# Optimization experiments

Hardware: AMD Instinct MI355X
Metric: run time of the kernel (lower is better)

The kernel has to match this reference:

```python
import jax, jax.numpy as jnp
import numpy as np
from jax.scipy.special import gammaln

N_L, N_Q, D_IN, D_CTX, H, MAX_AGENT = 256, 65536, 384, 192, 64, 6
STD2 = 0.1
VAR2 = STD2 * STD2
LOG_VAR2 = float(np.log(VAR2))
TEMP = 1.0


def _linear_init(k, out_dim, in_dim):
    k1, k2 = jax.random.split(k)
    s = 1.0 / np.sqrt(in_dim)
    w = jax.random.uniform(k1, (out_dim, in_dim), minval=-s, maxval=s, dtype=jnp.float32)
    b = jax.random.uniform(k2, (out_dim,), minval=-s, maxval=s, dtype=jnp.float32)
    return w, b


def setup_inputs() -> dict:
    key = jax.random.key(0)
    ks = jax.random.split(key, 12)
    fc1_w, fc1_b = _linear_init(ks[0], H, D_IN)
    fc21_w, fc21_b = _linear_init(ks[1], H, H)
    fc22_w, fc22_b = _linear_init(ks[2], H, H)
    fc3_w, fc3_b = _linear_init(ks[3], H, H)
    fc4_w, fc4_b = _linear_init(ks[4], D_IN, H)
    ctx_w, ctx_b = _linear_init(ks[5], H, D_CTX)
    llms = jax.random.normal(ks[6], (N_L, D_IN), dtype=jnp.float32)
    contexts = jax.random.normal(ks[7], (N_Q, D_CTX), dtype=jnp.float32)
    agent_num_int = jax.random.randint(ks[8], (N_Q, 1), 1, MAX_AGENT + 1, dtype=jnp.int32)
    agent_num_float = agent_num_int.astype(jnp.float32)
    noise_eps = jax.random.normal(ks[9], (N_L, H), dtype=jnp.float32)   # VAE reparameterize eps
    rand_u = jax.random.uniform(ks[10], (MAX_AGENT, N_Q, 1), dtype=jnp.float32)  # per-step uniforms
    return dict(llms=llms, contexts=contexts, agent_num_int=agent_num_int,
                agent_num_float=agent_num_float,
                fc1_w=fc1_w, fc1_b=fc1_b, fc21_w=fc21_w, fc21_b=fc21_b,
                fc22_w=fc22_w, fc22_b=fc22_b, fc3_w=fc3_w, fc3_b=fc3_b,
                fc4_w=fc4_w, fc4_b=fc4_b, ctx_w=ctx_w, ctx_b=ctx_b,
                noise_eps=noise_eps, rand_u=rand_u)


def _l2norm(x):
    n = jnp.sqrt(jnp.sum(x * x, axis=1, keepdims=True))
    return x / jnp.maximum(n, 1e-12)


def reference(llms, contexts, agent_num_int, agent_num_float,
              fc1_w, fc1_b, fc21_w, fc21_b, fc22_w, fc22_b,
              fc3_w, fc3_b, fc4_w, fc4_b, ctx_w, ctx_b, noise_eps, rand_u):
    # ---- VAE encode / reparameterize / decode ----
    h = jax.nn.relu(llms @ fc1_w.T + fc1_b)
    mu = h @ fc21_w.T + fc21_b
    log_var = h @ fc22_w.T + fc22_b
    std = jnp.exp(0.5 * log_var) * STD2
    z = mu + noise_eps * std
    h2 = jax.nn.relu(z @ fc3_w.T + fc3_b)
    x_hat = h2 @ fc4_w.T + fc4_b
    mse = jnp.mean((x_hat - llms) ** 2)
    kld = -0.5 * jnp.mean(1.0 - LOG_VAR2 + log_var - (mu ** 2 + jnp.exp(log_var)) / VAR2)
    vae_loss = mse + kld

    # ---- embeddings and routing scores ----
    llm_emb = _l2norm(z)                                   # [N_l, H]
    ctx_emb = _l2norm(contexts @ ctx_w.T + ctx_b)          # [N_q, H]
    scores = jax.nn.softmax((ctx_emb @ llm_emb.T) / TEMP, axis=1)  # [N_q, N_l]
    scores_cumsum = jnp.cumsum(scores, axis=1)

    # ---- vectorized max_agent-step categorical sampling ----
    # sel[i, q] = first llm where cumsum > u (inverse-CDF sampling), for step i
    sel = jnp.argmax(scores_cumsum[None, :, :] > rand_u, axis=2)          # [A, N_q]
    steps = jnp.arange(1, rand_u.shape[0] + 1, dtype=agent_num_int.dtype)
    mask = (agent_num_int[None, :, 0] >= steps[:, None]).astype(scores.dtype)  # [A, N_q]
    rows = jnp.broadcast_to(jnp.arange(scores.shape[0])[None, :], sel.shape)
    selected_llm = jnp.zeros_like(scores).at[rows, sel].add(mask)          # [N_q, N_l]

    log_probs = (gammaln(agent_num_float + 1.0)
                 - jnp.sum(gammaln(selected_llm + 1.0), axis=1, keepdims=True)
                 + jnp.sum(selected_llm * jnp.log(scores), axis=1, keepdims=True))
    return selected_llm, log_probs, vae_loss
```

## Files before the change

### kernel.cpp

```cpp
#include <hip/hip_runtime.h>
#include <hip/hip_bf16.h>

#define N_L 256
#define N_Q 65536
#define D_IN 384
#define D_CTX 192
#define HDIM 64
#define MAXA 6

__device__ __forceinline__ void fma4(float& acc, const float4& w, const float4& v) {
    acc = fmaf(w.x, v.x, acc);
    acc = fmaf(w.y, v.y, acc);
    acc = fmaf(w.z, v.z, acc);
    acc = fmaf(w.w, v.w, acc);
}

__device__ __forceinline__ float lgfact(int n) {
    return (n <= 1) ? 0.0f :
           (n == 2) ? 0.6931471805599453f :
           (n == 3) ? 1.7917594692280550f :
           (n == 4) ? 3.1780538303479458f :
           (n == 5) ? 4.7874917427820460f :
                      6.5792512120101010f;
}

__global__ __launch_bounds__(64) void vae_kernel(
    const float* __restrict__ llms, const float* __restrict__ ctx_w,
    const float* __restrict__ fc1_w, const float* __restrict__ fc1_b,
    const float* __restrict__ fc21_w, const float* __restrict__ fc21_b,
    const float* __restrict__ fc22_w, const float* __restrict__ fc22_b,
    const float* __restrict__ fc3_w, const float* __restrict__ fc3_b,
    const float* __restrict__ fc4_w, const float* __restrict__ fc4_b,
    const float* __restrict__ eps,
    float* __restrict__ ctx_wP, float* __restrict__ embT,
    float* __restrict__ mse_row, float* __restrict__ kld_row)
{
    __shared__ __align__(16) float xs[D_IN];
    __shared__ __align__(16) float hs[HDIM];
    __shared__ __align__(16) float zs[HDIM];
    __shared__ __align__(16) float h2s[HDIM];
    const int r = blockIdx.x;
    const int j = threadIdx.x;

    {
        int f = r * 64 + j;
        if (f < D_CTX * HDIM) {
            int p = f >> 2, rr = f & 3;
            int jc = p & 63, k4 = p >> 6;
            ctx_wP[f] = ctx_w[jc * D_CTX + k4 * 4 + rr];
        }
    }

    for (int k = j; k < D_IN; k += 64) xs[k] = llms[r * D_IN + k];
    __syncthreads();

    float acc = fc1_b[j];
    {
        const float4* wr = (const float4*)(fc1_w + (size_t)j * D_IN);
        const float4* xr = (const float4*)xs;
        #pragma unroll 8
        for (int k4 = 0; k4 < D_IN / 4; ++k4) { fma4(acc, wr[k4], xr[k4]); }
    }
    float h = fmaxf(acc, 0.0f);
    hs[j] = h;
    __syncthreads();

    float mu = fc21_b[j], lv = fc22_b[j];
    {
        const float4* w1 = (const float4*)(fc21_w + (size_t)j * HDIM);
        const float4* w2 = (const float4*)(fc22_w + (size_t)j * HDIM);
        const float4* hr = (const float4*)hs;
        #pragma unroll
        for (int k4 = 0; k4 < HDIM / 4; ++k4) {
            float4 hh = hr[k4];
            fma4(mu, w1[k4], hh);
            fma4(lv, w2[k4], hh);
        }
    }
    float stdv = expf(0.5f * lv) * 0.1f;
    float z = fmaf(eps[r * HDIM + j], stdv, mu);

    float elv = expf(lv);
    float kt = (1.0f - (-4.60517018598809136f)) + lv - (mu * mu + elv) / 0.01f;
    float ks = kt;
    #pragma unroll
    for (int o = 32; o; o >>= 1) ks += __shfl_xor(ks, o);

    float zsq = z * z;
    #pragma unroll
    for (int o = 32; o; o >>= 1) zsq += __shfl_xor(zsq, o);
    float nrm = fmaxf(sqrtf(zsq), 1e-12f);
    embT[j * N_L + r] = z / nrm;
    zs[j] = z;
    __syncthreads();

    float a3 = fc3_b[j];
    {
        const float4* w3 = (const float4*)(fc3_w + (size_t)j * HDIM);
        const float4* zr = (const float4*)zs;
        #pragma unroll
        for (int k4 = 0; k4 < HDIM / 4; ++k4) { fma4(a3, w3[k4], zr[k4]); }
    }
    float h2 = fmaxf(a3, 0.0f);
    h2s[j] = h2;
    __syncthreads();

    float ms = 0.0f;
    const float4* h2r = (const float4*)h2s;
    #pragma unroll
    for (int m = 0; m < 6; ++m) {
        int o = j + 64 * m;
        float a4 = fc4_b[o];
        const float4* w4 = (const float4*)(fc4_w + (size_t)o * HDIM);
        #pragma unroll
        for (int k4 = 0; k4 < HDIM / 4; ++k4) { fma4(a4, w4[k4], h2r[k4]); }
        float d = a4 - xs[o];
        ms = fmaf(d, d, ms);
    }
    #pragma unroll
    for (int o = 32; o; o >>= 1) ms += __shfl_xor(ms, o);
    if (j == 0) { mse_row[r] = ms; kld_row[r] = ks; }
}

__global__ __launch_bounds__(256) void route_kernel(
    const float* __restrict__ contexts, const float* __restrict__ ctx_wP, const float* __restrict__ ctx_b,
    const float* __restrict__ embT, const int* __restrict__ agent_num, const float* __restrict__ rand_u,
    const float* __restrict__ mse_row, const float* __restrict__ kld_row,
    float* __restrict__ out_sel, float* __restrict__ out_lp, float* __restrict__ out_loss)
{
    __shared__ __align__(16) float lds[4][1600];

    const int tid = threadIdx.x;
    const int lane = tid & 63;
    const int widx = tid >> 6;
    const int l0 = lane << 2;

    const int g = blockIdx.x * 4 + widx;
    const int q0 = __builtin_amdgcn_readfirstlane(g << 3);
    float* myl = lds[widx];

    {
        float4* xls = (float4*)myl;
        const float4* cbase = (const float4*)contexts + (size_t)q0 * (D_CTX / 4);
        #pragma unroll
        for (int it = 0; it < 6; ++it) {
            int f = lane + it * 64;
            xls[f] = cbase[f];
        }
        if (lane < 48)
            myl[1536 + lane] = rand_u[(lane >> 3) * N_Q + q0 + (lane & 7)];
    }

    if (g == 0) {
        int rr = lane * 4;
        float ms = mse_row[rr] + mse_row[rr + 1] + mse_row[rr + 2] + mse_row[rr + 3];
        float ks = kld_row[rr] + kld_row[rr + 1] + kld_row[rr + 2] + kld_row[rr + 3];
        #pragma unroll
        for (int o = 32; o; o >>= 1) { ms += __shfl_xor(ms, o); ks += __shfl_xor(ks, o); }
        if (lane == 0) out_loss[0] = ms / 98304.0f - 0.5f * (ks / 16384.0f);
    }

    int Aq[8];
    #pragma unroll
    for (int q = 0; q < 8; ++q)
        Aq[q] = __builtin_amdgcn_readfirstlane(agent_num[q0 + q]);

    const float bj = ctx_b[lane];
    float e[8];
    #pragma unroll
    for (int q = 0; q < 8; ++q) e[q] = bj;
    {
        const float4* wp = (const float4*)ctx_wP;
        const float4* xls = (const float4*)myl;
        #pragma unroll 2
        for (int k4 = 0; k4 < D_CTX / 4; ++k4) {
            float4 w = wp[k4 * HDIM + lane];
            #pragma unroll
            for (int q = 0; q < 8; ++q) {
                float4 xv = xls[q * 48 + k4];
                e[q] = fmaf(w.x, xv.x, e[q]);
                e[q] = fmaf(w.y, xv.y, e[q]);
                e[q] = fmaf(w.z, xv.z, e[q]);
                e[q] = fmaf(w.w, xv.w, e[q]);
            }
        }
    }
    {
        float s[8];
        #pragma unroll
        for (int q = 0; q < 8; ++q) s[q] = e[q] * e[q];
        #pragma unroll
        for (int o = 32; o; o >>= 1)
            #pragma unroll
            for (int q = 0; q < 8; ++q) s[q] += __shfl_xor(s[q], o);
        #pragma unroll
        for (int q = 0; q < 8; ++q) {
            e[q] *= 1.0f / fmaxf(sqrtf(s[q]), 1e-12f);
            myl[q * HDIM + lane] = e[q];
        }
    }

    float4 P[8];
    #pragma unroll
    for (int q = 0; q < 8; ++q) P[q] = make_float4(0.f, 0.f, 0.f, 0.f);

    #pragma unroll 2
    for (int j4 = 0; j4 < HDIM / 4; ++j4) {
        float4 M0 = *(const float4*)(embT + (size_t)(j4 * 4 + 0) * N_L + l0);
        float4 M1 = *(const float4*)(embT + (size_t)(j4 * 4 + 1) * N_L + l0);
        float4 M2 = *(const float4*)(embT + (size_t)(j4 * 4 + 2) * N_L + l0);
        float4 M3 = *(const float4*)(embT + (size_t)(j4 * 4 + 3) * N_L + l0);
        #pragma unroll
        for (int q = 0; q < 8; ++q) {
            float4 ev = *(const float4*)(myl + q * HDIM + j4 * 4);
            P[q].x = fmaf(M0.x, ev.x, P[q].x); P[q].x = fmaf(M1.x, ev.y, P[q].x);
            P[q].x = fmaf(M2.x, ev.z, P[q].x); P[q].x = fmaf(M3.x, ev.w, P[q].x);
            P[q].y = fmaf(M0.y, ev.x, P[q].y); P[q].y = fmaf(M1.y, ev.y, P[q].y);
            P[q].y = fmaf(M2.y, ev.z, P[q].y); P[q].y = fmaf(M3.y, ev.w, P[q].y);
            P[q].z = fmaf(M0.z, ev.x, P[q].z); P[q].z = fmaf(M1.z, ev.y, P[q].z);
            P[q].z = fmaf(M2.z, ev.z, P[q].z); P[q].z = fmaf(M3.z, ev.w, P[q].z);
            P[q].w = fmaf(M0.w, ev.x, P[q].w); P[q].w = fmaf(M1.w, ev.y, P[q].w);
            P[q].w = fmaf(M2.w, ev.z, P[q].w); P[q].w = fmaf(M3.w, ev.w, P[q].w);
        }
    }

    {
        float m[8], s[8];
        #pragma unroll
        for (int k = 0; k < 8; ++k) m[k] = fmaxf(fmaxf(P[k].x, P[k].y), fmaxf(P[k].z, P[k].w));
        #pragma unroll
        for (int o = 32; o; o >>= 1)
            #pragma unroll
            for (int k = 0; k < 8; ++k) m[k] = fmaxf(m[k], __shfl_xor(m[k], o));
        #pragma unroll
        for (int k = 0; k < 8; ++k) {
            P[k].x = expf(P[k].x - m[k]); P[k].y = expf(P[k].y - m[k]);
            P[k].z = expf(P[k].z - m[k]); P[k].w = expf(P[k].w - m[k]);
            s[k] = P[k].x + P[k].y + P[k].z + P[k].w;
        }
        #pragma unroll
        for (int o = 32; o; o >>= 1)
            #pragma unroll
            for (int k = 0; k < 8; ++k) s[k] += __shfl_xor(s[k], o);
        #pragma unroll
        for (int k = 0; k < 8; ++k) {
            float inv = 1.0f / s[k];
            P[k].x *= inv; P[k].y *= inv; P[k].z *= inv; P[k].w *= inv;
        }
    }

    float c0[8], c1[8], c2[8], c3[8];
    {
        float p3[8], t[8];
        #pragma unroll
        for (int k = 0; k < 8; ++k) {
            c0[k] = P[k].x; c1[k] = c0[k] + P[k].y; c2[k] = c1[k] + P[k].z; p3[k] = c2[k] + P[k].w;
            t[k] = p3[k];
        }
        #pragma unroll
        for (int o = 1; o < 64; o <<= 1)
            #pragma unroll
            for (int k = 0; k < 8; ++k) { float v = __shfl_up(t[k], o); if (lane >= o) t[k] += v; }
        #pragma unroll
        for (int k = 0; k < 8; ++k) {
            float base = t[k] - p3[k];
            c0[k] += base; c1[k] += base; c2[k] += base; c3[k] = p3[k] + base;
        }
    }

    unsigned nib[8] = {0, 0, 0, 0, 0, 0, 0, 0};
    #pragma unroll
    for (int i = 0; i < MAXA; ++i) {
        #pragma unroll
        for (int k = 0; k < 8; ++k) {
            if (i < Aq[k]) {
                float u = myl[1536 + i * 8 + k];
                unsigned long long b0 = __ballot(c0[k] <= u);
                unsigned long long b1 = __ballot(c1[k] <= u);
                unsigned long long b2 = __ballot(c2[k] <= u);
                unsigned long long b3 = __ballot(c3[k] <= u);
                int loc = __popcll(b0) + __popcll(b1) + __popcll(b2) + __popcll(b3);
                int sel = (loc >= N_L) ? 0 : loc;
                unsigned d = (unsigned)(sel - l0);
                if (d < 4u) nib[k] += 1u << (4 * d);
            }
        }
    }

    float term[8];
    #pragma unroll
    for (int k = 0; k < 8; ++k) {
        int n0 = nib[k] & 15, n1 = (nib[k] >> 4) & 15, n2 = (nib[k] >> 8) & 15, n3 = (nib[k] >> 12) & 15;
        float4 rowv = make_float4((float)n0, (float)n1, (float)n2, (float)n3);
        *(((float4*)(out_sel + (size_t)(q0 + k) * N_L)) + lane) = rowv;
        float tm = 0.0f;
        if (n0) tm += (float)n0 * logf(P[k].x) - lgfact(n0);
        if (n1) tm += (float)n1 * logf(P[k].y) - lgfact(n1);
        if (n2) tm += (float)n2 * logf(P[k].z) - lgfact(n2);
        if (n3) tm += (float)n3 * logf(P[k].w) - lgfact(n3);
        term[k] = tm;
    }
    #pragma unroll
    for (int o = 32; o; o >>= 1)
        #pragma unroll
        for (int k = 0; k < 8; ++k) term[k] += __shfl_xor(term[k], o);

    if (lane < 8) {
        float rr = term[0];
        int Aa = Aq[0];
        #pragma unroll
        for (int k = 1; k < 8; ++k) {
            if (lane == k) { rr = term[k]; Aa = Aq[k]; }
        }
        out_lp[q0 + lane] = lgfact(Aa) + rr;
    }
}

extern "C" void kernel_launch(void* const* d_in, const int* in_sizes, int n_in,
                              void* d_out, int out_size, void* d_ws, size_t ws_size,
                              hipStream_t stream) {
    const float* llms      = (const float*)d_in[0];
    const float* contexts  = (const float*)d_in[1];
    const int*   agent_i   = (const int*)  d_in[2];
    const float* fc1_w  = (const float*)d_in[4];  const float* fc1_b  = (const float*)d_in[5];
    const float* fc21_w = (const float*)d_in[6];  const float* fc21_b = (const float*)d_in[7];
    const float* fc22_w = (const float*)d_in[8];  const float* fc22_b = (const float*)d_in[9];
    const float* fc3_w  = (const float*)d_in[10]; const float* fc3_b  = (const float*)d_in[11];
    const float* fc4_w  = (const float*)d_in[12]; const float* fc4_b  = (const float*)d_in[13];
    const float* ctx_w  = (const float*)d_in[14]; const float* ctx_b  = (const float*)d_in[15];
    const float* noise  = (const float*)d_in[16]; const float* rand_u = (const float*)d_in[17];

    float* out      = (float*)d_out;
    float* out_sel  = out;
    float* out_lp   = out + (size_t)N_Q * N_L;
    float* out_loss = out_lp + N_Q;

    float* ctx_wP   = (float*)d_ws;
    float* embT     = ctx_wP + D_CTX * HDIM;
    float* mse_row  = embT + HDIM * N_L;
    float* kld_row  = mse_row + N_L;

    vae_kernel<<<N_L, 64, 0, stream>>>(llms, ctx_w, fc1_w, fc1_b, fc21_w, fc21_b, fc22_w, fc22_b,
                                       fc3_w, fc3_b, fc4_w, fc4_b, noise,
                                       ctx_wP, embT, mse_row, kld_row);
    route_kernel<<<2048, 256, 0, stream>>>(contexts, ctx_wP, ctx_b, embT, agent_i, rand_u,
                                           mse_row, kld_row, out_sel, out_lp, out_loss);
}
```

Before: 230.2 us.

## Use DPP wave scans, packed FP32 FMAs, and direct global loads in route kernel

```diff
diff --git a/kernel.cpp b/kernel.cpp
--- a/kernel.cpp
+++ b/kernel.cpp
@@ -1,5 +1,4 @@
 #include <hip/hip_runtime.h>
-#include <hip/hip_bf16.h>
 
 #define N_L 256
 #define N_Q 65536
@@ -7,6 +6,10 @@
 #define D_CTX 192
 #define HDIM 64
 #define MAXA 6
+
+typedef float v2f __attribute__((ext_vector_type(2)));
+
+__device__ __forceinline__ v2f mk2(float a, float b) { v2f r; r.x = a; r.y = b; return r; }
 
 __device__ __forceinline__ void fma4(float& acc, const float4& w, const float4& v) {
     acc = fmaf(w.x, v.x, acc);
@@ -22,6 +25,46 @@
            (n == 4) ? 3.1780538303479458f :
            (n == 5) ? 4.7874917427820460f :
                       6.5792512120101010f;
+}
+
+template<int CTRL, int RM, bool BC>
+__device__ __forceinline__ float dppz(float x) {
+    return __int_as_float(__builtin_amdgcn_update_dpp(0, __float_as_int(x), CTRL, RM, 0xF, BC));
+}
+template<int CTRL, int RM>
+__device__ __forceinline__ float dpps(float x) {
+    int xi = __float_as_int(x);
+    return __int_as_float(__builtin_amdgcn_update_dpp(xi, xi, CTRL, RM, 0xF, false));
+}
+__device__ __forceinline__ float wave_iscan(float t) {
+    t += dppz<0x111, 0xF, true>(t);
+    t += dppz<0x112, 0xF, true>(t);
+    t += dppz<0x114, 0xF, true>(t);
+    t += dppz<0x118, 0xF, true>(t);
+    t += dppz<0x142, 0xA, false>(t);
+    t += dppz<0x143, 0xC, false>(t);
+    return t;
+}
+__device__ __forceinline__ float wave_max_l63(float m) {
+    m = fmaxf(m, dpps<0x111, 0xF>(m));
+    m = fmaxf(m, dpps<0x112, 0xF>(m));
+    m = fmaxf(m, dpps<0x114, 0xF>(m));
+    m = fmaxf(m, dpps<0x118, 0xF>(m));
+    m = fmaxf(m, dpps<0x142, 0xA>(m));
+    m = fmaxf(m, dpps<0x143, 0xC>(m));
+    return m;
+}
+__device__ __forceinline__ float bc63(float x) {
+    return __int_as_float(__builtin_amdgcn_readlane(__float_as_int(x), 63));
+}
+
+__device__ __forceinline__ void pk_fma_lo(v2f& d, v2f a, v2f b) {
+    asm("v_pk_fma_f32 %0, %1, %2, %0 op_sel:[0,0,0] op_sel_hi:[1,0,1]"
+        : "+v"(d) : "v"(a), "v"(b));
+}
+__device__ __forceinline__ void pk_fma_hi(v2f& d, v2f a, v2f b) {
+    asm("v_pk_fma_f32 %0, %1, %2, %0 op_sel:[0,1,0] op_sel_hi:[1,1,1]"
+        : "+v"(d) : "v"(a), "v"(b));
 }
 
 __global__ __launch_bounds__(64) void vae_kernel(
@@ -128,7 +171,7 @@
     const float* __restrict__ mse_row, const float* __restrict__ kld_row,
     float* __restrict__ out_sel, float* __restrict__ out_lp, float* __restrict__ out_loss)
 {
-    __shared__ __align__(16) float lds[4][1600];
+    __shared__ __align__(16) float lds[4][512];
 
     const int tid = threadIdx.x;
     const int lane = tid & 63;
@@ -139,18 +182,6 @@
     const int q0 = __builtin_amdgcn_readfirstlane(g << 3);
     float* myl = lds[widx];
 
-    {
-        float4* xls = (float4*)myl;
-        const float4* cbase = (const float4*)contexts + (size_t)q0 * (D_CTX / 4);
-        #pragma unroll
-        for (int it = 0; it < 6; ++it) {
-            int f = lane + it * 64;
-            xls[f] = cbase[f];
-        }
-        if (lane < 48)
-            myl[1536 + lane] = rand_u[(lane >> 3) * N_Q + q0 + (lane & 7)];
-    }
-
     if (g == 0) {
         int rr = lane * 4;
         float ms = mse_row[rr] + mse_row[rr + 1] + mse_row[rr + 2] + mse_row[rr + 3];
@@ -162,47 +193,40 @@
 
     int Aq[8];
     #pragma unroll
-    for (int q = 0; q < 8; ++q)
-        Aq[q] = __builtin_amdgcn_readfirstlane(agent_num[q0 + q]);
+    for (int q = 0; q < 8; ++q) Aq[q] = agent_num[q0 + q];
 
     const float bj = ctx_b[lane];
-    float e[8];
-    #pragma unroll
-    for (int q = 0; q < 8; ++q) e[q] = bj;
+    v2f acc[8];
+    #pragma unroll
+    for (int q = 0; q < 8; ++q) acc[q] = mk2(bj, 0.0f);
     {
         const float4* wp = (const float4*)ctx_wP;
-        const float4* xls = (const float4*)myl;
+        const float4* xb = (const float4*)(contexts + (size_t)q0 * D_CTX);
         #pragma unroll 2
         for (int k4 = 0; k4 < D_CTX / 4; ++k4) {
             float4 w = wp[k4 * HDIM + lane];
+            v2f w01 = mk2(w.x, w.y), w23 = mk2(w.z, w.w);
             #pragma unroll
             for (int q = 0; q < 8; ++q) {
-                float4 xv = xls[q * 48 + k4];
-                e[q] = fmaf(w.x, xv.x, e[q]);
-                e[q] = fmaf(w.y, xv.y, e[q]);
-                e[q] = fmaf(w.z, xv.z, e[q]);
-                e[q] = fmaf(w.w, xv.w, e[q]);
+                float4 xv = xb[q * (D_CTX / 4) + k4];
+                acc[q] = __builtin_elementwise_fma(w01, mk2(xv.x, xv.y), acc[q]);
+                acc[q] = __builtin_elementwise_fma(w23, mk2(xv.z, xv.w), acc[q]);
             }
         }
     }
-    {
-        float s[8];
-        #pragma unroll
-        for (int q = 0; q < 8; ++q) s[q] = e[q] * e[q];
-        #pragma unroll
-        for (int o = 32; o; o >>= 1)
-            #pragma unroll
-            for (int q = 0; q < 8; ++q) s[q] += __shfl_xor(s[q], o);
-        #pragma unroll
-        for (int q = 0; q < 8; ++q) {
-            e[q] *= 1.0f / fmaxf(sqrtf(s[q]), 1e-12f);
-            myl[q * HDIM + lane] = e[q];
-        }
-    }
-
-    float4 P[8];
-    #pragma unroll
-    for (int q = 0; q < 8; ++q) P[q] = make_float4(0.f, 0.f, 0.f, 0.f);
+    float e[8];
+    #pragma unroll
+    for (int q = 0; q < 8; ++q) e[q] = acc[q].x + acc[q].y;
+    #pragma unroll
+    for (int q = 0; q < 8; ++q) {
+        float s = bc63(wave_iscan(e[q] * e[q]));
+        e[q] *= 1.0f / fmaxf(sqrtf(s), 1e-12f);
+        myl[q * HDIM + lane] = e[q];
+    }
+
+    v2f Pa[8], Pb[8];
+    #pragma unroll
+    for (int q = 0; q < 8; ++q) { Pa[q] = mk2(0.0f, 0.0f); Pb[q] = mk2(0.0f, 0.0f); }
 
     #pragma unroll 2
     for (int j4 = 0; j4 < HDIM / 4; ++j4) {
@@ -210,62 +234,48 @@
         float4 M1 = *(const float4*)(embT + (size_t)(j4 * 4 + 1) * N_L + l0);
         float4 M2 = *(const float4*)(embT + (size_t)(j4 * 4 + 2) * N_L + l0);
         float4 M3 = *(const float4*)(embT + (size_t)(j4 * 4 + 3) * N_L + l0);
+        v2f m0a = mk2(M0.x, M0.y), m0b = mk2(M0.z, M0.w);
+        v2f m1a = mk2(M1.x, M1.y), m1b = mk2(M1.z, M1.w);
+        v2f m2a = mk2(M2.x, M2.y), m2b = mk2(M2.z, M2.w);
+        v2f m3a = mk2(M3.x, M3.y), m3b = mk2(M3.z, M3.w);
         #pragma unroll
         for (int q = 0; q < 8; ++q) {
             float4 ev = *(const float4*)(myl + q * HDIM + j4 * 4);
-            P[q].x = fmaf(M0.x, ev.x, P[q].x); P[q].x = fmaf(M1.x, ev.y, P[q].x);
-            P[q].x = fmaf(M2.x, ev.z, P[q].x); P[q].x = fmaf(M3.x, ev.w, P[q].x);
-            P[q].y = fmaf(M0.y, ev.x, P[q].y); P[q].y = fmaf(M1.y, ev.y, P[q].y);
-            P[q].y = fmaf(M2.y, ev.z, P[q].y); P[q].y = fmaf(M3.y, ev.w, P[q].y);
-            P[q].z = fmaf(M0.z, ev.x, P[q].z); P[q].z = fmaf(M1.z, ev.y, P[q].z);
-            P[q].z = fmaf(M2.z, ev.z, P[q].z); P[q].z = fmaf(M3.z, ev.w, P[q].z);
-            P[q].w = fmaf(M0.w, ev.x, P[q].w); P[q].w = fmaf(M1.w, ev.y, P[q].w);
-            P[q].w = fmaf(M2.w, ev.z, P[q].w); P[q].w = fmaf(M3.w, ev.w, P[q].w);
-        }
-    }
-
-    {
-        float m[8], s[8];
-        #pragma unroll
-        for (int k = 0; k < 8; ++k) m[k] = fmaxf(fmaxf(P[k].x, P[k].y), fmaxf(P[k].z, P[k].w));
-        #pragma unroll
-        for (int o = 32; o; o >>= 1)
-            #pragma unroll
-            for (int k = 0; k < 8; ++k) m[k] = fmaxf(m[k], __shfl_xor(m[k], o));
-        #pragma unroll
-        for (int k = 0; k < 8; ++k) {
-            P[k].x = expf(P[k].x - m[k]); P[k].y = expf(P[k].y - m[k]);
-            P[k].z = expf(P[k].z - m[k]); P[k].w = expf(P[k].w - m[k]);
-            s[k] = P[k].x + P[k].y + P[k].z + P[k].w;
-        }
-        #pragma unroll
-        for (int o = 32; o; o >>= 1)
-            #pragma unroll
-            for (int k = 0; k < 8; ++k) s[k] += __shfl_xor(s[k], o);
-        #pragma unroll
-        for (int k = 0; k < 8; ++k) {
-            float inv = 1.0f / s[k];
-            P[k].x *= inv; P[k].y *= inv; P[k].z *= inv; P[k].w *= inv;
-        }
+            v2f e01 = mk2(ev.x, ev.y), e23 = mk2(ev.z, ev.w);
+            pk_fma_lo(Pa[q], m0a, e01);
+            pk_fma_hi(Pa[q], m1a, e01);
+            pk_fma_lo(Pa[q], m2a, e23);
+            pk_fma_hi(Pa[q], m3a, e23);
+            pk_fma_lo(Pb[q], m0b, e01);
+            pk_fma_hi(Pb[q], m1b, e01);
+            pk_fma_lo(Pb[q], m2b, e23);
+            pk_fma_hi(Pb[q], m3b, e23);
+        }
+    }
+
+    float4 P[8];
+    #pragma unroll
+    for (int k = 0; k < 8; ++k) P[k] = make_float4(Pa[k].x, Pa[k].y, Pb[k].x, Pb[k].y);
+
+    #pragma unroll
+    for (int k = 0; k < 8; ++k) {
+        float m = fmaxf(fmaxf(P[k].x, P[k].y), fmaxf(P[k].z, P[k].w));
+        m = bc63(wave_max_l63(m));
+        P[k].x = expf(P[k].x - m); P[k].y = expf(P[k].y - m);
+        P[k].z = expf(P[k].z - m); P[k].w = expf(P[k].w - m);
+        float s = bc63(wave_iscan(P[k].x + P[k].y + P[k].z + P[k].w));
+        float inv = 1.0f / s;
+        P[k].x *= inv; P[k].y *= inv; P[k].z *= inv; P[k].w *= inv;
     }
 
     float c0[8], c1[8], c2[8], c3[8];
-    {
-        float p3[8], t[8];
-        #pragma unroll
-        for (int k = 0; k < 8; ++k) {
-            c0[k] = P[k].x; c1[k] = c0[k] + P[k].y; c2[k] = c1[k] + P[k].z; p3[k] = c2[k] + P[k].w;
-            t[k] = p3[k];
-        }
-        #pragma unroll
-        for (int o = 1; o < 64; o <<= 1)
-            #pragma unroll
-            for (int k = 0; k < 8; ++k) { float v = __shfl_up(t[k], o); if (lane >= o) t[k] += v; }
-        #pragma unroll
-        for (int k = 0; k < 8; ++k) {
-            float base = t[k] - p3[k];
-            c0[k] += base; c1[k] += base; c2[k] += base; c3[k] = p3[k] + base;
-        }
+    #pragma unroll
+    for (int k = 0; k < 8; ++k) {
+        c0[k] = P[k].x; c1[k] = c0[k] + P[k].y; c2[k] = c1[k] + P[k].z;
+        float p3 = c2[k] + P[k].w;
+        float t = wave_iscan(p3);
+        float base = t - p3;
+        c0[k] += base; c1[k] += base; c2[k] += base; c3[k] = p3 + base;
     }
 
     unsigned nib[8] = {0, 0, 0, 0, 0, 0, 0, 0};
@@ -274,7 +284,7 @@
         #pragma unroll
         for (int k = 0; k < 8; ++k) {
             if (i < Aq[k]) {
-                float u = myl[1536 + i * 8 + k];
+                float u = rand_u[(size_t)i * N_Q + q0 + k];
                 unsigned long long b0 = __ballot(c0[k] <= u);
                 unsigned long long b1 = __ballot(c1[k] <= u);
                 unsigned long long b2 = __ballot(c2[k] <= u);
@@ -300,17 +310,16 @@
         if (n3) tm += (float)n3 * logf(P[k].w) - lgfact(n3);
         term[k] = tm;
     }
-    #pragma unroll
-    for (int o = 32; o; o >>= 1)
-        #pragma unroll
-        for (int k = 0; k < 8; ++k) term[k] += __shfl_xor(term[k], o);
+    float st[8];
+    #pragma unroll
+    for (int k = 0; k < 8; ++k) st[k] = bc63(wave_iscan(term[k]));
 
     if (lane < 8) {
-        float rr = term[0];
+        float rr = st[0];
         int Aa = Aq[0];
         #pragma unroll
         for (int k = 1; k < 8; ++k) {
-            if (lane == k) { rr = term[k]; Aa = Aq[k]; }
+            if (lane == k) { rr = st[k]; Aa = Aq[k]; }
         }
         out_lp[q0 + lane] = lgfact(Aa) + rr;
     }
```

Result: slower. 258.6 us (+12.3%).
